# Kernel tuning notes

Measured on AMD Instinct MI355X. Metric: run time of the kernel, lower is better.

## Reference

```python
import jax, jax.numpy as jnp
import numpy as np
from jax import lax

N, CIN, H, W = 16, 3, 512, 512
BH = BW = 16  # block size (h, w); bstride == bsize so blocks tile the image
EPS = 1e-5


def setup_inputs() -> dict:
    key = jax.random.key(0)
    ks = jax.random.split(key, 32)
    def nrm(k, shape, s=0.05):
        return jax.random.normal(k, shape, jnp.float32) * s
    def bnp(k, ch):
        # rows: gamma, beta, running_mean, running_var (var kept > 0)
        u = jax.random.uniform(k, (4, ch), jnp.float32)
        return u.at[3].add(0.1)
    feat = (H // 4) * (W // 4) * 8
    return {
        "x": jax.random.normal(ks[0], (N, CIN, H, W), jnp.float32),
        "mask": jax.random.uniform(ks[1], (N, 1, H, W), jnp.float32),
        "s1_cw": nrm(ks[2], (16, CIN, 1, 1)), "s1_cb": nrm(ks[3], (16,)), "s1_bn0": bnp(ks[4], 16),
        "s1_d1w": nrm(ks[5], (32, 16, 1, 1)), "s1_d1b": nrm(ks[6], (32,)), "s1_bn1": bnp(ks[7], 32),
        "s1_d2w": nrm(ks[8], (32, 32, 3, 3)), "s1_d2b": nrm(ks[9], (32,)), "s1_bn2": bnp(ks[10], 32),
        "s1_d3w": nrm(ks[11], (16, 32, 1, 1)), "s1_d3b": nrm(ks[12], (16,)), "s1_bn3": bnp(ks[13], 16),
        "s2_cw": nrm(ks[14], (8, 16, 1, 1)), "s2_cb": nrm(ks[15], (8,)), "s2_bn0": bnp(ks[16], 8),
        "s2_d1w": nrm(ks[17], (16, 8, 1, 1)), "s2_d1b": nrm(ks[18], (16,)), "s2_bn1": bnp(ks[19], 16),
        "s2_d2w": nrm(ks[20], (16, 16, 3, 3)), "s2_d2b": nrm(ks[21], (16,)), "s2_bn2": bnp(ks[22], 16),
        "s2_d3w": nrm(ks[23], (8, 16, 1, 1)), "s2_d3b": nrm(ks[24], (8,)), "s2_bn3": bnp(ks[25], 8),
        "fc_w": nrm(ks[26], (10, feat), 0.01), "fc_b": nrm(ks[27], (10,)),
    }


def conv(x, w, b, p):
    y = lax.conv_general_dilated(x, w, (1, 1), [(p, p), (p, p)],
                                 dimension_numbers=("NCHW", "OIHW", "NCHW"))
    return y + b[None, :, None, None]


def bnorm(x, p):
    g, bt, m, v = p[0], p[1], p[2], p[3]
    scale = g * lax.rsqrt(v + EPS)
    return scale[None, :, None, None] * (x - m[None, :, None, None]) + bt[None, :, None, None]


def to_blocks(x):
    # [N,C,H,W] -> [N*nby*nbx, C, BH, BW]
    n, c, hh, ww = x.shape
    nby, nbx = hh // BH, ww // BW
    b = x.reshape(n, c, nby, BH, nbx, BW).transpose(0, 2, 4, 1, 3, 5)
    return b.reshape(n * nby * nbx, c, BH, BW), (n, nby, nbx)


def from_blocks(b, meta, c):
    n, nby, nbx = meta
    x = b.reshape(n, nby, nbx, c, BH, BW).transpose(0, 3, 1, 4, 2, 5)
    return x.reshape(n, c, nby * BH, nbx * BW)


def maxpool2(x):
    return lax.reduce_window(x, -jnp.inf, lax.max, (1, 1, 2, 2), (1, 1, 2, 2), "VALID")


def sparse_conv_block(x, mask, cw, cb, bn0, d1w, d1b, bn1, d2w, d2b, bn2, d3w, d3b, bn3):
    # reduce_mask: block is active if its mean mask value exceeds threshold
    mblocks, _ = to_blocks(mask)
    active = mblocks.mean(axis=(1, 2, 3)) > 0.5  # [N*nblocks]
    # channel path (applies to every pixel)
    xc = bnorm(jax.nn.relu(conv(x, cw, cb, 0)), bn0)
    # gather -> dense bottleneck convs per block (3x3 padded within each block) -> scatter
    blocks, meta = to_blocks(xc)
    g = bnorm(jax.nn.relu(conv(blocks, d1w, d1b, 0)), bn1)
    g = bnorm(jax.nn.relu(conv(g, d2w, d2b, 1)), bn2)
    g = bnorm(jax.nn.relu(conv(g, d3w, d3b, 0)), bn3)
    out = jnp.where(active[:, None, None, None], g, blocks)
    return from_blocks(out, meta, xc.shape[1])


def reference(x, mask, s1_cw, s1_cb, s1_bn0, s1_d1w, s1_d1b, s1_bn1, s1_d2w, s1_d2b, s1_bn2,
              s1_d3w, s1_d3b, s1_bn3, s2_cw, s2_cb, s2_bn0, s2_d1w, s2_d1b, s2_bn1,
              s2_d2w, s2_d2b, s2_bn2, s2_d3w, s2_d3b, s2_bn3, fc_w, fc_b):
    x1 = sparse_conv_block(x, mask, s1_cw, s1_cb, s1_bn0, s1_d1w, s1_d1b, s1_bn1,
                           s1_d2w, s1_d2b, s1_bn2, s1_d3w, s1_d3b, s1_bn3)
    x1 = maxpool2(x1)
    mask2 = maxpool2(mask)
    x2 = sparse_conv_block(x1, mask2, s2_cw, s2_cb, s2_bn0, s2_d1w, s2_d1b, s2_bn1,
                           s2_d2w, s2_d2b, s2_bn2, s2_d3w, s2_d3b, s2_bn3)
    x2 = maxpool2(x2)
    flat = x2.reshape(x2.shape[0], -1)  # [N, (H/4)*(W/4)*8]
    logits = flat @ fc_w.T + fc_b
    return jax.nn.softmax(logits, axis=-1)
```

## Files before the change

### kernel.cpp

```cpp
#include <hip/hip_runtime.h>
#include <math.h>


typedef __attribute__((ext_vector_type(8))) short bf16x8;
typedef __attribute__((ext_vector_type(4))) float f32x4;

#define X1P_OFF 0
#define X2_OFF  16777216
#define LG_OFF  18874368
#define P_OFF   18874624

enum : int {
  WT_S1C  = 0,
  WT_S2C  = 48,
  SC_S1BN0 = 176,
  SC_S1BN1 = 208,
  SC_S1BN2 = 272,
  SC_S1BN3 = 336,
  SC_S2BN0 = 368,
  SC_S2BN1 = 384,
  SC_S2BN2 = 416,
  SC_S2BN3 = 448,
  PH_F     = 464
};
enum : int {
  H_S1D2 = 0,
  H_S1D3 = 9216,
  H_S2D2 = 9728,
  H_S2D3 = 12288,
  H_S1D1 = 12544,
  H_S2D1 = 13568,
  PH_END = 14080
};

__device__ __forceinline__ float relu_f(float v) { return v > 0.f ? v : 0.f; }

__device__ __forceinline__ unsigned short f2bf(float f) {
  unsigned int u = __float_as_uint(f);
  unsigned int r = (u + 0x7fffu + ((u >> 16) & 1u)) >> 16;
  return (unsigned short)r;
}

__device__ __forceinline__ unsigned int pk2(float lo, float hi) {
  unsigned int r;
  asm("v_cvt_pk_bf16_f32 %0, %1, %2" : "=v"(r) : "v"(lo), "v"(hi));
  return r;
}

__device__ __forceinline__ void prep_bn(const float* __restrict__ p, int C,
                                        float* __restrict__ dst, int t) {
  for (int i = t; i < C; i += 256) {
    float g = p[i], b = p[C + i], m = p[2 * C + i], v = p[3 * C + i];
    float s = g / sqrtf(v + 1e-5f);
    dst[i] = s;
    dst[C + i] = b - s * m;
  }
}

__global__ __launch_bounds__(256) void prep_kernel(
    const float* __restrict__ s1_cw, const float* __restrict__ s1_d1w,
    const float* __restrict__ s1_d2w, const float* __restrict__ s1_d3w,
    const float* __restrict__ s2_cw, const float* __restrict__ s2_d1w,
    const float* __restrict__ s2_d2w, const float* __restrict__ s2_d3w,
    const float* __restrict__ s1_bn0, const float* __restrict__ s1_bn1,
    const float* __restrict__ s1_bn2, const float* __restrict__ s1_bn3,
    const float* __restrict__ s2_bn0, const float* __restrict__ s2_bn1,
    const float* __restrict__ s2_bn2, const float* __restrict__ s2_bn3,
    float* __restrict__ P, float* __restrict__ lg) {
  const int t = threadIdx.x;
  unsigned short* PH = (unsigned short*)(P + PH_F);
  for (int i = t; i < 48;  i += 256) { int co = i / 3,  ci = i % 3;  P[WT_S1C + ci * 16 + co] = s1_cw[i]; }
  for (int i = t; i < 128; i += 256) { int co = i / 16, ci = i % 16; P[WT_S2C + ci * 8  + co] = s2_cw[i]; }
  for (int i = t; i < 9216; i += 256) {
    int tap = i >> 10, o = (i >> 5) & 31, ci = i & 31;
    PH[H_S1D2 + i] = f2bf(s1_d2w[o * 288 + ci * 9 + tap]);
  }
  for (int i = t; i < 512; i += 256) PH[H_S1D3 + i] = f2bf(s1_d3w[i]);
  for (int i = t; i < 2560; i += 256) {
    int p = i >> 9, o = (i >> 5) & 15, k = i & 31;
    int tp = 2 * p + (k >> 4);
    PH[H_S2D2 + i] = (tp < 9) ? f2bf(s2_d2w[o * 144 + (k & 15) * 9 + tp]) : 0;
  }
  for (int i = t; i < 256; i += 256) {
    int nn = i >> 4, k = i & 15;
    PH[H_S2D3 + i] = (nn < 8) ? f2bf(s2_d3w[nn * 16 + k]) : 0;
  }
  for (int i = t; i < 1024; i += 256) {
    int o = i >> 5, k = i & 31;
    PH[H_S1D1 + i] = (k < 16) ? f2bf(s1_d1w[o * 16 + k]) : 0;
  }
  for (int i = t; i < 512; i += 256) {
    int o = i >> 5, k = i & 31;
    PH[H_S2D1 + i] = (k < 8) ? f2bf(s2_d1w[o * 8 + k]) : 0;
  }
  prep_bn(s1_bn0, 16, P + SC_S1BN0, t);
  prep_bn(s1_bn1, 32, P + SC_S1BN1, t);
  prep_bn(s1_bn2, 32, P + SC_S1BN2, t);
  prep_bn(s1_bn3, 16, P + SC_S1BN3, t);
  prep_bn(s2_bn0, 8,  P + SC_S2BN0, t);
  prep_bn(s2_bn1, 16, P + SC_S2BN1, t);
  prep_bn(s2_bn2, 16, P + SC_S2BN2, t);
  prep_bn(s2_bn3, 8,  P + SC_S2BN3, t);
  if (t < 160) lg[t] = 0.f;
}

__global__ __launch_bounds__(256, 3) void stage1_kernel(
    const float* __restrict__ x, const float* __restrict__ mask,
    const float* __restrict__ cbv, const float* __restrict__ d1b,
    const float* __restrict__ d2b, const float* __restrict__ d3b,
    const float* __restrict__ P, float* __restrict__ x1p) {
  __shared__ __align__(16) unsigned char ldsb[25920];
  __shared__ float red[4];
  __shared__ int actflag;

  const int t = threadIdx.x;
  const int ty = t >> 4, tx = t & 15;
  const int b = blockIdx.x;
  const int n = b >> 10;
  const int by = (b >> 5) & 31, bx = b & 31;
  const int gy = by * 16 + ty, gx = bx * 16 + tx;

  float s = mask[(size_t)(n * 512 + gy) * 512 + gx];
  #pragma unroll
  for (int off = 32; off > 0; off >>= 1) s += __shfl_down(s, off, 64);
  if ((t & 63) == 0) red[t >> 6] = s;
  __syncthreads();
  if (t == 0) actflag = (red[0] + red[1] + red[2] + red[3]) > 128.0f;
  __syncthreads();
  const bool active = (actflag != 0);

  float xin[3];
  #pragma unroll
  for (int c = 0; c < 3; ++c)
    xin[c] = x[(size_t)((n * 3 + c) * 512 + gy) * 512 + gx];

  const float* wc = P + WT_S1C;
  const float* sc0 = P + SC_S1BN0;
  float xc[16];
  {
    float a[16];
    #pragma unroll
    for (int o = 0; o < 16; ++o) a[o] = cbv[o];
    #pragma unroll
    for (int c = 0; c < 3; ++c) {
      const float v = xin[c];
      #pragma unroll
      for (int o = 0; o < 16; ++o) a[o] = fmaf(wc[c * 16 + o], v, a[o]);
    }
    #pragma unroll
    for (int o = 0; o < 16; ++o) xc[o] = fmaf(sc0[o], relu_f(a[o]), sc0[16 + o]);
  }

  float* const poolf = (float*)(ldsb + 20480);

  if (active) {
    const int w = t >> 6, lane = t & 63;
    const int lr = lane & 15, cb = lane >> 4;
    const unsigned short* PH = (const unsigned short*)(P + PH_F);

    if (t < 68) {
      int row, col;
      if (t < 18)      { row = 0;      col = t;      }
      else if (t < 36) { row = 17;     col = t - 18; }
      else if (t < 52) { row = t - 35; col = 0;      }
      else             { row = t - 51; col = 17;     }
      uint4* z = (uint4*)(ldsb + (row * 18 + col) * 80);
      const uint4 z4 = make_uint4(0u, 0u, 0u, 0u);
      z[0] = z4; z[1] = z4; z[2] = z4; z[3] = z4;
    }
    {
      unsigned int pk[8];
      #pragma unroll
      for (int i = 0; i < 8; ++i) pk[i] = pk2(xc[2 * i], xc[2 * i + 1]);
      uint4* dst = (uint4*)(ldsb + ((ty + 1) * 18 + (tx + 1)) * 80);
      dst[0] = make_uint4(pk[0], pk[1], pk[2], pk[3]);
      dst[1] = make_uint4(pk[4], pk[5], pk[6], pk[7]);
    }

    bf16x8 w1f[2];
    #pragma unroll
    for (int ct = 0; ct < 2; ++ct)
      w1f[ct] = *(const bf16x8*)(PH + H_S1D1 + (ct * 16 + lr) * 32 + cb * 8);
    f32x4 acc1[2][4];
    #pragma unroll
    for (int ct = 0; ct < 2; ++ct) {
      const float4 bb = *(const float4*)(d1b + ct * 16 + cb * 4);
      #pragma unroll
      for (int nt = 0; nt < 4; ++nt) {
        acc1[ct][nt][0] = bb.x; acc1[ct][nt][1] = bb.y;
        acc1[ct][nt][2] = bb.z; acc1[ct][nt][3] = bb.w;
      }
    }
    #pragma unroll
    for (int nt = 0; nt < 4; ++nt) {
      bf16x8 xcf;
      if (cb < 2) xcf = *(const bf16x8*)(ldsb + ((w * 4 + nt + 1) * 18 + lr + 1) * 80 + cb * 16);
      else        xcf = (bf16x8)(short)0;
      #pragma unroll
      for (int ct = 0; ct < 2; ++ct)
        acc1[ct][nt] = __builtin_amdgcn_mfma_f32_16x16x32_bf16(w1f[ct], xcf, acc1[ct][nt], 0, 0, 0);
    }
    #pragma unroll
    for (int ct = 0; ct < 2; ++ct) {
      const float4 s1s = *(const float4*)(P + SC_S1BN1 + ct * 16 + cb * 4);
      const float4 s1h = *(const float4*)(P + SC_S1BN1 + 32 + ct * 16 + cb * 4);
      #pragma unroll
      for (int nt = 0; nt < 4; ++nt) {
        const unsigned base = ((w * 4 + nt + 1) * 18 + lr + 1) * 80 + (ct * 16 + cb * 4) * 2;
        *(unsigned int*)(ldsb + base) =
            pk2(fmaf(s1s.x, relu_f(acc1[ct][nt][0]), s1h.x),
                fmaf(s1s.y, relu_f(acc1[ct][nt][1]), s1h.y));
        *(unsigned int*)(ldsb + base + 4) =
            pk2(fmaf(s1s.z, relu_f(acc1[ct][nt][2]), s1h.z),
                fmaf(s1s.w, relu_f(acc1[ct][nt][3]), s1h.w));
      }
    }
    __syncthreads();

    const int ct3 = w & 1, ph = w >> 1;
    bf16x8 bw[9];
    #pragma unroll
    for (int tap = 0; tap < 9; ++tap)
      bw[tap] = *(const bf16x8*)(PH + H_S1D2 + (tap * 32 + ct3 * 16 + lr) * 32 + cb * 8);
    f32x4 acc2[8];
    {
      const float4 bb = *(const float4*)(d2b + ct3 * 16 + cb * 4);
      #pragma unroll
      for (int q = 0; q < 8; ++q) {
        acc2[q][0] = bb.x; acc2[q][1] = bb.y; acc2[q][2] = bb.z; acc2[q][3] = bb.w;
      }
    }
    #pragma unroll
    for (int tap = 0; tap < 9; ++tap) {
      const int dy = tap / 3, dx = tap % 3;
      #pragma unroll
      for (int q = 0; q < 8; ++q) {
        const bf16x8 af = *(const bf16x8*)(ldsb + ((ph * 8 + q + dy) * 18 + lr + dx) * 80 + cb * 16);
        acc2[q] = __builtin_amdgcn_mfma_f32_16x16x32_bf16(bw[tap], af, acc2[q], 0, 0, 0);
      }
    }
    __syncthreads();

    {
      const float4 s2s = *(const float4*)(P + SC_S1BN2 + ct3 * 16 + cb * 4);
      const float4 s2h = *(const float4*)(P + SC_S1BN2 + 32 + ct3 * 16 + cb * 4);
      #pragma unroll
      for (int q = 0; q < 8; ++q) {
        const int pix = (ph * 8 + q) * 16 + lr;
        const unsigned base = pix * 80 + (ct3 * 16 + cb * 4) * 2;
        *(unsigned int*)(ldsb + base) =
            pk2(fmaf(s2s.x, relu_f(acc2[q][0]), s2h.x),
                fmaf(s2s.y, relu_f(acc2[q][1]), s2h.y));
        *(unsigned int*)(ldsb + base + 4) =
            pk2(fmaf(s2s.z, relu_f(acc2[q][2]), s2h.z),
                fmaf(s2s.w, relu_f(acc2[q][3]), s2h.w));
      }
    }
    __syncthreads();

    const bf16x8 b3 = *(const bf16x8*)(PH + H_S1D3 + lr * 32 + cb * 8);
    const float bias3v = d3b[lr];
    const float sc3v = P[SC_S1BN3 + lr], sh3v = P[SC_S1BN3 + 16 + lr];
    f32x4 acc3[4];
    #pragma unroll
    for (int mt = 0; mt < 4; ++mt) {
      acc3[mt][0] = bias3v; acc3[mt][1] = bias3v; acc3[mt][2] = bias3v; acc3[mt][3] = bias3v;
      const bf16x8 a3 = *(const bf16x8*)(ldsb + (w * 64 + mt * 16 + lr) * 80 + cb * 16);
      acc3[mt] = __builtin_amdgcn_mfma_f32_16x16x32_bf16(a3, b3, acc3[mt], 0, 0, 0);
    }
    #pragma unroll
    for (int mtp = 0; mtp < 2; ++mtp) {
      float o0[4], o1[4];
      #pragma unroll
      for (int r = 0; r < 4; ++r) {
        o0[r] = fmaf(sc3v, relu_f(acc3[2 * mtp][r]), sh3v);
        o1[r] = fmaf(sc3v, relu_f(acc3[2 * mtp + 1][r]), sh3v);
      }
      #pragma unroll
      for (int rp = 0; rp < 2; ++rp) {
        const float m = fmaxf(fmaxf(o0[2 * rp], o0[2 * rp + 1]),
                              fmaxf(o1[2 * rp], o1[2 * rp + 1]));
        poolf[lr * 68 + (w * 2 + mtp) * 8 + cb * 2 + rp] = m;
      }
    }
  } else {
    float* ldsf = (float*)ldsb;
    {
      float* pw = &ldsf[t * 20];
      #pragma unroll
      for (int c = 0; c < 16; ++c) pw[c] = xc[c];
    }
    __syncthreads();
    {
      const int pp = t & 63, cg = t >> 6;
      const int py = pp >> 3, px = pp & 7;
      const float* r0 = &ldsf[((2 * py) * 16 + 2 * px) * 20 + cg * 4];
      const float* r2 = &ldsf[((2 * py + 1) * 16 + 2 * px) * 20 + cg * 4];
      const float4 v0 = *(const float4*)(r0);
      const float4 v1 = *(const float4*)(r0 + 20);
      const float4 v2 = *(const float4*)(r2);
      const float4 v3 = *(const float4*)(r2 + 20);
      poolf[(cg * 4 + 0) * 68 + py * 8 + px] = fmaxf(fmaxf(v0.x, v1.x), fmaxf(v2.x, v3.x));
      poolf[(cg * 4 + 1) * 68 + py * 8 + px] = fmaxf(fmaxf(v0.y, v1.y), fmaxf(v2.y, v3.y));
      poolf[(cg * 4 + 2) * 68 + py * 8 + px] = fmaxf(fmaxf(v0.z, v1.z), fmaxf(v2.z, v3.z));
      poolf[(cg * 4 + 3) * 68 + py * 8 + px] = fmaxf(fmaxf(v0.w, v1.w), fmaxf(v2.w, v3.w));
    }
  }

  __syncthreads();
  {
    const int ch = t >> 4, idx = t & 15, yy = idx >> 1, h = idx & 1;
    const uint4 v = *(const uint4*)(poolf + ch * 68 + yy * 8 + h * 4);
    const size_t ob = ((((size_t)n * 16 + (by >> 1)) * 16 + (bx >> 1)) * 16 + ch) * 256
                      + (size_t)((by & 1) * 8 + yy) * 16 + (bx & 1) * 8 + h * 4;
    *(uint4*)(x1p + ob) = v;
  }
}

__global__ __launch_bounds__(256, 4) void stage2_kernel(
    const float* __restrict__ mask,
    const float* __restrict__ cbv, const float* __restrict__ d1b,
    const float* __restrict__ d2b, const float* __restrict__ d3b,
    const float* __restrict__ P, const float* __restrict__ x1p,
    float* __restrict__ x2) {
  __shared__ __align__(16) unsigned char ldsb2[15552];
  __shared__ float red[4];
  __shared__ int actflag;

  const int t = threadIdx.x;
  const int ty = t >> 4, tx = t & 15;
  const int b = blockIdx.x;
  const int n = b >> 8;
  const int BY = (b >> 4) & 15, BX = b & 15;

  const int my = (BY * 16 + ty) * 2, mx = (BX * 16 + tx) * 2;
  const float* mp = &mask[(size_t)(n * 512 + my) * 512 + mx];
  float s = fmaxf(fmaxf(mp[0], mp[1]), fmaxf(mp[512], mp[513]));
  #pragma unroll
  for (int off = 32; off > 0; off >>= 1) s += __shfl_down(s, off, 64);
  if ((t & 63) == 0) red[t >> 6] = s;
  __syncthreads();
  if (t == 0) actflag = (red[0] + red[1] + red[2] + red[3]) > 128.0f;
  __syncthreads();
  const bool active = (actflag != 0);

  const float* xb = x1p + (size_t)((n * 16 + BY) * 16 + BX) * 4096 + ty * 16 + tx;
  float xin[16];
  #pragma unroll
  for (int c = 0; c < 16; ++c) xin[c] = xb[c * 256];

  const float* wc = P + WT_S2C;
  const float* sc0 = P + SC_S2BN0;
  float xc[8];
  {
    float a[8];
    #pragma unroll
    for (int o = 0; o < 8; ++o) a[o] = cbv[o];
    #pragma unroll
    for (int c = 0; c < 16; ++c) {
      const float v = xin[c];
      #pragma unroll
      for (int o = 0; o < 8; ++o) a[o] = fmaf(wc[c * 8 + o], v, a[o]);
    }
    #pragma unroll
    for (int o = 0; o < 8; ++o) xc[o] = fmaf(sc0[o], relu_f(a[o]), sc0[8 + o]);
  }

  float* const poolf = (float*)(ldsb2 + 12288);

  if (active) {
    const int w = t >> 6, lane = t & 63;
    const int lr = lane & 15, cb = lane >> 4;
    const unsigned short* PH = (const unsigned short*)(P + PH_F);

    if (t < 68) {
      int row, col;
      if (t < 18)      { row = 0;      col = t;      }
      else if (t < 36) { row = 17;     col = t - 18; }
      else if (t < 52) { row = t - 35; col = 0;      }
      else             { row = t - 51; col = 17;     }
      uint4* z = (uint4*)(ldsb2 + (row * 18 + col) * 48);
      const uint4 z4 = make_uint4(0u, 0u, 0u, 0u);
      z[0] = z4; z[1] = z4;
    }
    {
      unsigned int pk[4];
      #pragma unroll
      for (int i = 0; i < 4; ++i) pk[i] = pk2(xc[2 * i], xc[2 * i + 1]);
      *(uint4*)(ldsb2 + ((ty + 1) * 18 + (tx + 1)) * 48) = make_uint4(pk[0], pk[1], pk[2], pk[3]);
    }

    const bf16x8 w1f = *(const bf16x8*)(PH + H_S2D1 + lr * 32 + cb * 8);
    f32x4 acc1[4];
    {
      const float4 bb = *(const float4*)(d1b + cb * 4);
      #pragma unroll
      for (int nt = 0; nt < 4; ++nt) {
        acc1[nt][0] = bb.x; acc1[nt][1] = bb.y; acc1[nt][2] = bb.z; acc1[nt][3] = bb.w;
      }
    }
    #pragma unroll
    for (int nt = 0; nt < 4; ++nt) {
      bf16x8 xcf;
      if (cb == 0) xcf = *(const bf16x8*)(ldsb2 + ((w * 4 + nt + 1) * 18 + lr + 1) * 48);
      else         xcf = (bf16x8)(short)0;
      acc1[nt] = __builtin_amdgcn_mfma_f32_16x16x32_bf16(w1f, xcf, acc1[nt], 0, 0, 0);
    }
    {
      const float4 s1s = *(const float4*)(P + SC_S2BN1 + cb * 4);
      const float4 s1h = *(const float4*)(P + SC_S2BN1 + 16 + cb * 4);
      #pragma unroll
      for (int nt = 0; nt < 4; ++nt) {
        const unsigned base = ((w * 4 + nt + 1) * 18 + lr + 1) * 48 + cb * 8;
        *(unsigned int*)(ldsb2 + base) =
            pk2(fmaf(s1s.x, relu_f(acc1[nt][0]), s1h.x),
                fmaf(s1s.y, relu_f(acc1[nt][1]), s1h.y));
        *(unsigned int*)(ldsb2 + base + 4) =
            pk2(fmaf(s1s.z, relu_f(acc1[nt][2]), s1h.z),
                fmaf(s1s.w, relu_f(acc1[nt][3]), s1h.w));
      }
    }
    __syncthreads();

    bf16x8 bw2[5];
    #pragma unroll
    for (int p = 0; p < 5; ++p)
      bw2[p] = *(const bf16x8*)(PH + H_S2D2 + (p * 16 + lr) * 32 + cb * 8);
    f32x4 acc2[4];
    {
      const float4 bb = *(const float4*)(d2b + cb * 4);
      #pragma unroll
      for (int nt = 0; nt < 4; ++nt) {
        acc2[nt][0] = bb.x; acc2[nt][1] = bb.y; acc2[nt][2] = bb.z; acc2[nt][3] = bb.w;
      }
    }
    #pragma unroll
    for (int p = 0; p < 5; ++p) {
      const int tp = (p < 4) ? (2 * p + (cb >> 1)) : 8;
      const int dy = (tp >= 6) ? 2 : ((tp >= 3) ? 1 : 0);
      const int dx = tp - dy * 3;
      #pragma unroll
      for (int nt = 0; nt < 4; ++nt) {
        const bf16x8 af = *(const bf16x8*)(ldsb2 + ((w * 4 + nt + dy) * 18 + lr + dx) * 48 + (cb & 1) * 16);
        acc2[nt] = __builtin_amdgcn_mfma_f32_16x16x32_bf16(bw2[p], af, acc2[nt], 0, 0, 0);
      }
    }
    __syncthreads();

    {
      const float4 s2s = *(const float4*)(P + SC_S2BN2 + cb * 4);
      const float4 s2h = *(const float4*)(P + SC_S2BN2 + 16 + cb * 4);
      #pragma unroll
      for (int nt = 0; nt < 4; ++nt) {
        const int pix = w * 64 + nt * 16 + lr;
        const unsigned base = pix * 48 + cb * 8;
        *(unsigned int*)(ldsb2 + base) =
            pk2(fmaf(s2s.x, relu_f(acc2[nt][0]), s2h.x),
                fmaf(s2s.y, relu_f(acc2[nt][1]), s2h.y));
        *(unsigned int*)(ldsb2 + base + 4) =
            pk2(fmaf(s2s.z, relu_f(acc2[nt][2]), s2h.z),
                fmaf(s2s.w, relu_f(acc2[nt][3]), s2h.w));
      }
    }
    __syncthreads();

    bf16x8 b3;
    if (cb < 2) b3 = *(const bf16x8*)(PH + H_S2D3 + lr * 16 + cb * 8);
    else        b3 = (bf16x8)(short)0;
    const float bias3v = (lr < 8) ? d3b[lr] : 0.f;
    const float sc3v = (lr < 8) ? P[SC_S2BN3 + lr] : 0.f;
    const float sh3v = (lr < 8) ? P[SC_S2BN3 + 8 + lr] : 0.f;
    f32x4 acc3[4];
    #pragma unroll
    for (int mt = 0; mt < 4; ++mt) {
      acc3[mt][0] = bias3v; acc3[mt][1] = bias3v; acc3[mt][2] = bias3v; acc3[mt][3] = bias3v;
      bf16x8 a3;
      if (cb < 2) a3 = *(const bf16x8*)(ldsb2 + (w * 64 + mt * 16 + lr) * 48 + cb * 16);
      else        a3 = (bf16x8)(short)0;
      acc3[mt] = __builtin_amdgcn_mfma_f32_16x16x32_bf16(a3, b3, acc3[mt], 0, 0, 0);
    }
    if (lr < 8) {
      #pragma unroll
      for (int mtp = 0; mtp < 2; ++mtp) {
        float o0[4], o1[4];
        #pragma unroll
        for (int r = 0; r < 4; ++r) {
          o0[r] = fmaf(sc3v, relu_f(acc3[2 * mtp][r]), sh3v);
          o1[r] = fmaf(sc3v, relu_f(acc3[2 * mtp + 1][r]), sh3v);
        }
        #pragma unroll
        for (int rp = 0; rp < 2; ++rp) {
          const float m = fmaxf(fmaxf(o0[2 * rp], o0[2 * rp + 1]),
                                fmaxf(o1[2 * rp], o1[2 * rp + 1]));
          poolf[lr * 68 + (w * 2 + mtp) * 8 + cb * 2 + rp] = m;
        }
      }
    }
  } else {
    float* ldsf = (float*)ldsb2;
    {
      float* pw = &ldsf[t * 12];
      #pragma unroll
      for (int c = 0; c < 8; ++c) pw[c] = xc[c];
    }
    __syncthreads();
    if (t < 128) {
      const int pp = t & 63, cg = t >> 6;
      const int py = pp >> 3, px = pp & 7;
      const float* r0 = &ldsf[((2 * py) * 16 + 2 * px) * 12 + cg * 4];
      const float* r2 = &ldsf[((2 * py + 1) * 16 + 2 * px) * 12 + cg * 4];
      const float4 v0 = *(const float4*)(r0);
      const float4 v1 = *(const float4*)(r0 + 12);
      const float4 v2 = *(const float4*)(r2);
      const float4 v3 = *(const float4*)(r2 + 12);
      poolf[(cg * 4 + 0) * 68 + py * 8 + px] = fmaxf(fmaxf(v0.x, v1.x), fmaxf(v2.x, v3.x));
      poolf[(cg * 4 + 1) * 68 + py * 8 + px] = fmaxf(fmaxf(v0.y, v1.y), fmaxf(v2.y, v3.y));
      poolf[(cg * 4 + 2) * 68 + py * 8 + px] = fmaxf(fmaxf(v0.z, v1.z), fmaxf(v2.z, v3.z));
      poolf[(cg * 4 + 3) * 68 + py * 8 + px] = fmaxf(fmaxf(v0.w, v1.w), fmaxf(v2.w, v3.w));
    }
  }

  __syncthreads();
  if (t < 128) {
    const int ch = t >> 4, idx = t & 15, yy = idx >> 1, h = idx & 1;
    const uint4 v = *(const uint4*)(poolf + ch * 68 + yy * 8 + h * 4);
    const size_t ob = ((size_t)(n * 8 + ch) * 128 + (BY * 8 + yy)) * 128 + BX * 8 + h * 4;
    *(uint4*)(x2 + ob) = v;
  }
}

__global__ __launch_bounds__(256) void fc_kernel(const float* __restrict__ x2,
                                                 const float* __restrict__ fcw,
                                                 const float* __restrict__ fcb,
                                                 float* __restrict__ logits) {
  __shared__ float red[4];
  const int wg = blockIdx.x, t = threadIdx.x;
  const int sp = wg & 7, k = (wg >> 3) % 10, n = wg / 80;
  const float4* xa = (const float4*)(x2 + (size_t)n * 131072) + sp * 4096;
  const float4* wa = (const float4*)(fcw + (size_t)k * 131072) + sp * 4096;
  float s = 0.f;
  #pragma unroll 4
  for (int i = t; i < 4096; i += 256) {
    const float4 a = xa[i], b = wa[i];
    s = fmaf(a.x, b.x, fmaf(a.y, b.y, fmaf(a.z, b.z, fmaf(a.w, b.w, s))));
  }
  #pragma unroll
  for (int off = 32; off > 0; off >>= 1) s += __shfl_down(s, off, 64);
  if ((t & 63) == 0) red[t >> 6] = s;
  __syncthreads();
  if (t == 0) {
    float tot = red[0] + red[1] + red[2] + red[3];
    if (sp == 0) tot += fcb[k];
    atomicAdd(&logits[n * 10 + k], tot);
  }
}

__global__ void softmax_kernel(const float* __restrict__ logits, float* __restrict__ out) {
  const int t = threadIdx.x;
  if (t < 16) {
    float l[10], mx = -1e30f;
    #pragma unroll
    for (int k = 0; k < 10; ++k) { l[k] = logits[t * 10 + k]; mx = fmaxf(mx, l[k]); }
    float sum = 0.f;
    #pragma unroll
    for (int k = 0; k < 10; ++k) { l[k] = expf(l[k] - mx); sum += l[k]; }
    const float inv = 1.f / sum;
    #pragma unroll
    for (int k = 0; k < 10; ++k) out[t * 10 + k] = l[k] * inv;
  }
}

extern "C" void kernel_launch(void* const* d_in, const int* in_sizes, int n_in,
                              void* d_out, int out_size, void* d_ws, size_t ws_size,
                              hipStream_t stream) {
  const float* x      = (const float*)d_in[0];
  const float* mask   = (const float*)d_in[1];
  const float* s1_cw  = (const float*)d_in[2];
  const float* s1_cb  = (const float*)d_in[3];
  const float* s1_bn0 = (const float*)d_in[4];
  const float* s1_d1w = (const float*)d_in[5];
  const float* s1_d1b = (const float*)d_in[6];
  const float* s1_bn1 = (const float*)d_in[7];
  const float* s1_d2w = (const float*)d_in[8];
  const float* s1_d2b = (const float*)d_in[9];
  const float* s1_bn2 = (const float*)d_in[10];
  const float* s1_d3w = (const float*)d_in[11];
  const float* s1_d3b = (const float*)d_in[12];
  const float* s1_bn3 = (const float*)d_in[13];
  const float* s2_cw  = (const float*)d_in[14];
  const float* s2_cb  = (const float*)d_in[15];
  const float* s2_bn0 = (const float*)d_in[16];
  const float* s2_d1w = (const float*)d_in[17];
  const float* s2_d1b = (const float*)d_in[18];
  const float* s2_bn1 = (const float*)d_in[19];
  const float* s2_d2w = (const float*)d_in[20];
  const float* s2_d2b = (const float*)d_in[21];
  const float* s2_bn2 = (const float*)d_in[22];
  const float* s2_d3w = (const float*)d_in[23];
  const float* s2_d3b = (const float*)d_in[24];
  const float* s2_bn3 = (const float*)d_in[25];
  const float* fc_w   = (const float*)d_in[26];
  const float* fc_b   = (const float*)d_in[27];

  float* ws  = (float*)d_ws;
  float* x1p = ws + X1P_OFF;
  float* x2  = ws + X2_OFF;
  float* lg  = ws + LG_OFF;
  float* P   = ws + P_OFF;

  prep_kernel<<<1, 256, 0, stream>>>(s1_cw, s1_d1w, s1_d2w, s1_d3w,
                                     s2_cw, s2_d1w, s2_d2w, s2_d3w,
                                     s1_bn0, s1_bn1, s1_bn2, s1_bn3,
                                     s2_bn0, s2_bn1, s2_bn2, s2_bn3, P, lg);
  stage1_kernel<<<16 * 32 * 32, 256, 0, stream>>>(x, mask, s1_cb, s1_d1b, s1_d2b, s1_d3b, P, x1p);
  stage2_kernel<<<16 * 16 * 16, 256, 0, stream>>>(mask, s2_cb, s2_d1b, s2_d2b, s2_d3b, P, x1p, x2);
  fc_kernel<<<1280, 256, 0, stream>>>(x2, fc_w, fc_b, lg);
  softmax_kernel<<<1, 64, 0, stream>>>(lg, (float*)d_out);
}
```

Baseline: 295.4 us.

## Precompute stage-2 activity sums in stage 1 and cut register pressure for occupancy

Stage 1 now also computes the 2x2-maxpooled mask sum for each stage-2 block and accumulates it with atomics into a small buffer zeroed by the prep kernel. Stage 2 reads that one value instead of re-reading the mask and running its own block reduction and two barriers. The 3x3 conv weight loads are moved inside non-unrolled per-row (stage 1) and per-pair (stage 2) loops, and launch bounds are raised to 4 and 5 blocks per CU. The cost is fewer live registers and higher occupancy, traded for repeated weight loads inside the loop, atomics, and less unrolling.

```diff
diff --git a/kernel.cpp b/kernel.cpp
--- a/kernel.cpp
+++ b/kernel.cpp
@@ -8,7 +8,8 @@
 #define X1P_OFF 0
 #define X2_OFF  16777216
 #define LG_OFF  18874368
-#define P_OFF   18874624
+#define MS_OFF  18874624
+#define P_OFF   18878720
 
 enum : int {
   WT_S1C  = 0,
@@ -66,7 +67,7 @@
     const float* __restrict__ s1_bn2, const float* __restrict__ s1_bn3,
     const float* __restrict__ s2_bn0, const float* __restrict__ s2_bn1,
     const float* __restrict__ s2_bn2, const float* __restrict__ s2_bn3,
-    float* __restrict__ P, float* __restrict__ lg) {
+    float* __restrict__ P, float* __restrict__ lg, float* __restrict__ ms) {
   const int t = threadIdx.x;
   unsigned short* PH = (unsigned short*)(P + PH_F);
   for (int i = t; i < 48;  i += 256) { int co = i / 3,  ci = i % 3;  P[WT_S1C + ci * 16 + co] = s1_cw[i]; }
@@ -102,16 +103,17 @@
   prep_bn(s2_bn2, 16, P + SC_S2BN2, t);
   prep_bn(s2_bn3, 8,  P + SC_S2BN3, t);
   if (t < 160) lg[t] = 0.f;
-}
-
-__global__ __launch_bounds__(256, 3) void stage1_kernel(
+  for (int i = t; i < 4096; i += 256) ms[i] = 0.f;
+}
+
+__global__ __launch_bounds__(256, 4) void stage1_kernel(
     const float* __restrict__ x, const float* __restrict__ mask,
     const float* __restrict__ cbv, const float* __restrict__ d1b,
     const float* __restrict__ d2b, const float* __restrict__ d3b,
-    const float* __restrict__ P, float* __restrict__ x1p) {
+    const float* __restrict__ P, float* __restrict__ x1p,
+    float* __restrict__ msum) {
   __shared__ __align__(16) unsigned char ldsb[25920];
-  __shared__ float red[4];
-  __shared__ int actflag;
+  __shared__ float red_s[4], red_v[4];
 
   const int t = threadIdx.x;
   const int ty = t >> 4, tx = t & 15;
@@ -120,14 +122,19 @@
   const int by = (b >> 5) & 31, bx = b & 31;
   const int gy = by * 16 + ty, gx = bx * 16 + tx;
 
-  float s = mask[(size_t)(n * 512 + gy) * 512 + gx];
-  #pragma unroll
-  for (int off = 32; off > 0; off >>= 1) s += __shfl_down(s, off, 64);
-  if ((t & 63) == 0) red[t >> 6] = s;
+  {
+    const float m = mask[(size_t)(n * 512 + gy) * 512 + gx];
+    float v = fmaxf(m, __shfl_xor(m, 1, 64));
+    v = fmaxf(v, __shfl_xor(v, 16, 64));
+    float s = m;
+    #pragma unroll
+    for (int off = 32; off > 0; off >>= 1) {
+      s += __shfl_down(s, off, 64);
+      v += __shfl_down(v, off, 64);
+    }
+    if ((t & 63) == 0) { red_s[t >> 6] = s; red_v[t >> 6] = v; }
+  }
   __syncthreads();
-  if (t == 0) actflag = (red[0] + red[1] + red[2] + red[3]) > 128.0f;
-  __syncthreads();
-  const bool active = (actflag != 0);
 
   float xin[3];
   #pragma unroll
@@ -150,6 +157,11 @@
     #pragma unroll
     for (int o = 0; o < 16; ++o) xc[o] = fmaf(sc0[o], relu_f(a[o]), sc0[16 + o]);
   }
+
+  const bool active = (red_s[0] + red_s[1] + red_s[2] + red_s[3]) > 128.0f;
+  if (t == 0)
+    atomicAdd(&msum[n * 256 + (by >> 1) * 16 + (bx >> 1)],
+              (red_v[0] + red_v[1] + red_v[2] + red_v[3]) * 0.25f);
 
   float* const poolf = (float*)(ldsb + 20480);
 
@@ -177,51 +189,49 @@
       dst[1] = make_uint4(pk[4], pk[5], pk[6], pk[7]);
     }
 
-    bf16x8 w1f[2];
-    #pragma unroll
-    for (int ct = 0; ct < 2; ++ct)
-      w1f[ct] = *(const bf16x8*)(PH + H_S1D1 + (ct * 16 + lr) * 32 + cb * 8);
-    f32x4 acc1[2][4];
-    #pragma unroll
-    for (int ct = 0; ct < 2; ++ct) {
-      const float4 bb = *(const float4*)(d1b + ct * 16 + cb * 4);
+    {
+      bf16x8 w1f[2];
+      #pragma unroll
+      for (int ct = 0; ct < 2; ++ct)
+        w1f[ct] = *(const bf16x8*)(PH + H_S1D1 + (ct * 16 + lr) * 32 + cb * 8);
+      f32x4 acc1[2][4];
+      #pragma unroll
+      for (int ct = 0; ct < 2; ++ct) {
+        const float4 bb = *(const float4*)(d1b + ct * 16 + cb * 4);
+        #pragma unroll
+        for (int nt = 0; nt < 4; ++nt) {
+          acc1[ct][nt][0] = bb.x; acc1[ct][nt][1] = bb.y;
+          acc1[ct][nt][2] = bb.z; acc1[ct][nt][3] = bb.w;
+        }
+      }
       #pragma unroll
       for (int nt = 0; nt < 4; ++nt) {
-        acc1[ct][nt][0] = bb.x; acc1[ct][nt][1] = bb.y;
-        acc1[ct][nt][2] = bb.z; acc1[ct][nt][3] = bb.w;
-      }
-    }
-    #pragma unroll
-    for (int nt = 0; nt < 4; ++nt) {
-      bf16x8 xcf;
-      if (cb < 2) xcf = *(const bf16x8*)(ldsb + ((w * 4 + nt + 1) * 18 + lr + 1) * 80 + cb * 16);
-      else        xcf = (bf16x8)(short)0;
-      #pragma unroll
-      for (int ct = 0; ct < 2; ++ct)
-        acc1[ct][nt] = __builtin_amdgcn_mfma_f32_16x16x32_bf16(w1f[ct], xcf, acc1[ct][nt], 0, 0, 0);
-    }
-    #pragma unroll
-    for (int ct = 0; ct < 2; ++ct) {
-      const float4 s1s = *(const float4*)(P + SC_S1BN1 + ct * 16 + cb * 4);
-      const float4 s1h = *(const float4*)(P + SC_S1BN1 + 32 + ct * 16 + cb * 4);
-      #pragma unroll
-      for (int nt = 0; nt < 4; ++nt) {
-        const unsigned base = ((w * 4 + nt + 1) * 18 + lr + 1) * 80 + (ct * 16 + cb * 4) * 2;
-        *(unsigned int*)(ldsb + base) =
-            pk2(fmaf(s1s.x, relu_f(acc1[ct][nt][0]), s1h.x),
-                fmaf(s1s.y, relu_f(acc1[ct][nt][1]), s1h.y));
-        *(unsigned int*)(ldsb + base + 4) =
-            pk2(fmaf(s1s.z, relu_f(acc1[ct][nt][2]), s1h.z),
-                fmaf(s1s.w, relu_f(acc1[ct][nt][3]), s1h.w));
+        bf16x8 xcf;
+        if (cb < 2) xcf = *(const bf16x8*)(ldsb + ((w * 4 + nt + 1) * 18 + lr + 1) * 80 + cb * 16);
+        else        xcf = (bf16x8)(short)0;
+        #pragma unroll
+        for (int ct = 0; ct < 2; ++ct)
+          acc1[ct][nt] = __builtin_amdgcn_mfma_f32_16x16x32_bf16(w1f[ct], xcf, acc1[ct][nt], 0, 0, 0);
+      }
+      #pragma unroll
+      for (int ct = 0; ct < 2; ++ct) {
+        const float4 s1s = *(const float4*)(P + SC_S1BN1 + ct * 16 + cb * 4);
+        const float4 s1h = *(const float4*)(P + SC_S1BN1 + 32 + ct * 16 + cb * 4);
+        #pragma unroll
+        for (int nt = 0; nt < 4; ++nt) {
+          const unsigned base = ((w * 4 + nt + 1) * 18 + lr + 1) * 80 + (ct * 16 + cb * 4) * 2;
+          *(unsigned int*)(ldsb + base) =
+              pk2(fmaf(s1s.x, relu_f(acc1[ct][nt][0]), s1h.x),
+                  fmaf(s1s.y, relu_f(acc1[ct][nt][1]), s1h.y));
+          *(unsigned int*)(ldsb + base + 4) =
+              pk2(fmaf(s1s.z, relu_f(acc1[ct][nt][2]), s1h.z),
+                  fmaf(s1s.w, relu_f(acc1[ct][nt][3]), s1h.w));
+        }
       }
     }
     __syncthreads();
 
     const int ct3 = w & 1, ph = w >> 1;
-    bf16x8 bw[9];
-    #pragma unroll
-    for (int tap = 0; tap < 9; ++tap)
-      bw[tap] = *(const bf16x8*)(PH + H_S1D2 + (tap * 32 + ct3 * 16 + lr) * 32 + cb * 8);
     f32x4 acc2[8];
     {
       const float4 bb = *(const float4*)(d2b + ct3 * 16 + cb * 4);
@@ -230,14 +240,20 @@
         acc2[q][0] = bb.x; acc2[q][1] = bb.y; acc2[q][2] = bb.z; acc2[q][3] = bb.w;
       }
     }
-    #pragma unroll
-    for (int tap = 0; tap < 9; ++tap) {
-      const int dy = tap / 3, dx = tap % 3;
-      #pragma unroll
-      for (int q = 0; q < 8; ++q) {
-        const bf16x8 af = *(const bf16x8*)(ldsb + ((ph * 8 + q + dy) * 18 + lr + dx) * 80 + cb * 16);
-        acc2[q] = __builtin_amdgcn_mfma_f32_16x16x32_bf16(bw[tap], af, acc2[q], 0, 0, 0);
-      }
+    #pragma clang loop unroll(disable)
+    for (int dy = 0; dy < 3; ++dy) {
+      bf16x8 bwr[3];
+      #pragma unroll
+      for (int dx = 0; dx < 3; ++dx)
+        bwr[dx] = *(const bf16x8*)(PH + H_S1D2 + ((dy * 3 + dx) * 32 + ct3 * 16 + lr) * 32 + cb * 8);
+      const int rb = (ph * 8 + dy) * 18 + lr;
+      #pragma unroll
+      for (int dx = 0; dx < 3; ++dx)
+        #pragma unroll
+        for (int q = 0; q < 8; ++q) {
+          const bf16x8 af = *(const bf16x8*)(ldsb + (rb + q * 18 + dx) * 80 + cb * 16);
+          acc2[q] = __builtin_amdgcn_mfma_f32_16x16x32_bf16(bwr[dx], af, acc2[q], 0, 0, 0);
+        }
     }
     __syncthreads();
 
@@ -317,15 +333,13 @@
   }
 }
 
-__global__ __launch_bounds__(256, 4) void stage2_kernel(
-    const float* __restrict__ mask,
+__global__ __launch_bounds__(256, 5) void stage2_kernel(
+    const float* __restrict__ msum,
     const float* __restrict__ cbv, const float* __restrict__ d1b,
     const float* __restrict__ d2b, const float* __restrict__ d3b,
     const float* __restrict__ P, const float* __restrict__ x1p,
     float* __restrict__ x2) {
   __shared__ __align__(16) unsigned char ldsb2[15552];
-  __shared__ float red[4];
-  __shared__ int actflag;
 
   const int t = threadIdx.x;
   const int ty = t >> 4, tx = t & 15;
@@ -333,18 +347,9 @@
   const int n = b >> 8;
   const int BY = (b >> 4) & 15, BX = b & 15;
 
-  const int my = (BY * 16 + ty) * 2, mx = (BX * 16 + tx) * 2;
-  const float* mp = &mask[(size_t)(n * 512 + my) * 512 + mx];
-  float s = fmaxf(fmaxf(mp[0], mp[1]), fmaxf(mp[512], mp[513]));
-  #pragma unroll
-  for (int off = 32; off > 0; off >>= 1) s += __shfl_down(s, off, 64);
-  if ((t & 63) == 0) red[t >> 6] = s;
-  __syncthreads();
-  if (t == 0) actflag = (red[0] + red[1] + red[2] + red[3]) > 128.0f;
-  __syncthreads();
-  const bool active = (actflag != 0);
-
-  const float* xb = x1p + (size_t)((n * 16 + BY) * 16 + BX) * 4096 + ty * 16 + tx;
+  const bool active = msum[b] > 128.0f;
+
+  const float* xb = x1p + (size_t)b * 4096 + ty * 16 + tx;
   float xin[16];
   #pragma unroll
   for (int c = 0; c < 16; ++c) xin[c] = xb[c * 256];
@@ -390,42 +395,40 @@
       *(uint4*)(ldsb2 + ((ty + 1) * 18 + (tx + 1)) * 48) = make_uint4(pk[0], pk[1], pk[2], pk[3]);
     }
 
-    const bf16x8 w1f = *(const bf16x8*)(PH + H_S2D1 + lr * 32 + cb * 8);
-    f32x4 acc1[4];
-    {
-      const float4 bb = *(const float4*)(d1b + cb * 4);
+    {
+      const bf16x8 w1f = *(const bf16x8*)(PH + H_S2D1 + lr * 32 + cb * 8);
+      f32x4 acc1[4];
+      {
+        const float4 bb = *(const float4*)(d1b + cb * 4);
+        #pragma unroll
+        for (int nt = 0; nt < 4; ++nt) {
+          acc1[nt][0] = bb.x; acc1[nt][1] = bb.y; acc1[nt][2] = bb.z; acc1[nt][3] = bb.w;
+        }
+      }
       #pragma unroll
       for (int nt = 0; nt < 4; ++nt) {
-        acc1[nt][0] = bb.x; acc1[nt][1] = bb.y; acc1[nt][2] = bb.z; acc1[nt][3] = bb.w;
-      }
-    }
-    #pragma unroll
-    for (int nt = 0; nt < 4; ++nt) {
-      bf16x8 xcf;
-      if (cb == 0) xcf = *(const bf16x8*)(ldsb2 + ((w * 4 + nt + 1) * 18 + lr + 1) * 48);
-      else         xcf = (bf16x8)(short)0;
-      acc1[nt] = __builtin_amdgcn_mfma_f32_16x16x32_bf16(w1f, xcf, acc1[nt], 0, 0, 0);
-    }
-    {
-      const float4 s1s = *(const float4*)(P + SC_S2BN1 + cb * 4);
-      const float4 s1h = *(const float4*)(P + SC_S2BN1 + 16 + cb * 4);
-      #pragma unroll
-      for (int nt = 0; nt < 4; ++nt) {
-        const unsigned base = ((w * 4 + nt + 1) * 18 + lr + 1) * 48 + cb * 8;
-        *(unsigned int*)(ldsb2 + base) =
-            pk2(fmaf(s1s.x, relu_f(acc1[nt][0]), s1h.x),
-                fmaf(s1s.y, relu_f(acc1[nt][1]), s1h.y));
-        *(unsigned int*)(ldsb2 + base + 4) =
-            pk2(fmaf(s1s.z, relu_f(acc1[nt][2]), s1h.z),
-                fmaf(s1s.w, relu_f(acc1[nt][3]), s1h.w));
-      }
-    }
-    __syncthreads();
-
-    bf16x8 bw2[5];
-    #pragma unroll
-    for (int p = 0; p < 5; ++p)
-      bw2[p] = *(const bf16x8*)(PH + H_S2D2 + (p * 16 + lr) * 32 + cb * 8);
+        bf16x8 xcf;
+        if (cb == 0) xcf = *(const bf16x8*)(ldsb2 + ((w * 4 + nt + 1) * 18 + lr + 1) * 48);
+        else         xcf = (bf16x8)(short)0;
+        acc1[nt] = __builtin_amdgcn_mfma_f32_16x16x32_bf16(w1f, xcf, acc1[nt], 0, 0, 0);
+      }
+      {
+        const float4 s1s = *(const float4*)(P + SC_S2BN1 + cb * 4);
+        const float4 s1h = *(const float4*)(P + SC_S2BN1 + 16 + cb * 4);
+        #pragma unroll
+        for (int nt = 0; nt < 4; ++nt) {
+          const unsigned base = ((w * 4 + nt + 1) * 18 + lr + 1) * 48 + cb * 8;
+          *(unsigned int*)(ldsb2 + base) =
+              pk2(fmaf(s1s.x, relu_f(acc1[nt][0]), s1h.x),
+                  fmaf(s1s.y, relu_f(acc1[nt][1]), s1h.y));
+          *(unsigned int*)(ldsb2 + base + 4) =
+              pk2(fmaf(s1s.z, relu_f(acc1[nt][2]), s1h.z),
+                  fmaf(s1s.w, relu_f(acc1[nt][3]), s1h.w));
+        }
+      }
+    }
+    __syncthreads();
+
     f32x4 acc2[4];
     {
       const float4 bb = *(const float4*)(d2b + cb * 4);
@@ -434,15 +437,16 @@
         acc2[nt][0] = bb.x; acc2[nt][1] = bb.y; acc2[nt][2] = bb.z; acc2[nt][3] = bb.w;
       }
     }
-    #pragma unroll
+    #pragma clang loop unroll(disable)
     for (int p = 0; p < 5; ++p) {
+      const bf16x8 bwp = *(const bf16x8*)(PH + H_S2D2 + (p * 16 + lr) * 32 + cb * 8);
       const int tp = (p < 4) ? (2 * p + (cb >> 1)) : 8;
       const int dy = (tp >= 6) ? 2 : ((tp >= 3) ? 1 : 0);
       const int dx = tp - dy * 3;
       #pragma unroll
       for (int nt = 0; nt < 4; ++nt) {
         const bf16x8 af = *(const bf16x8*)(ldsb2 + ((w * 4 + nt + dy) * 18 + lr + dx) * 48 + (cb & 1) * 16);
-        acc2[nt] = __builtin_amdgcn_mfma_f32_16x16x32_bf16(bw2[p], af, acc2[nt], 0, 0, 0);
+        acc2[nt] = __builtin_amdgcn_mfma_f32_16x16x32_bf16(bwp, af, acc2[nt], 0, 0, 0);
       }
     }
     __syncthreads();
@@ -606,14 +610,15 @@
   float* x1p = ws + X1P_OFF;
   float* x2  = ws + X2_OFF;
   float* lg  = ws + LG_OFF;
+  float* ms  = ws + MS_OFF;
   float* P   = ws + P_OFF;
 
   prep_kernel<<<1, 256, 0, stream>>>(s1_cw, s1_d1w, s1_d2w, s1_d3w,
                                      s2_cw, s2_d1w, s2_d2w, s2_d3w,
                                      s1_bn0, s1_bn1, s1_bn2, s1_bn3,
-                                     s2_bn0, s2_bn1, s2_bn2, s2_bn3, P, lg);
-  stage1_kernel<<<16 * 32 * 32, 256, 0, stream>>>(x, mask, s1_cb, s1_d1b, s1_d2b, s1_d3b, P, x1p);
-  stage2_kernel<<<16 * 16 * 16, 256, 0, stream>>>(mask, s2_cb, s2_d1b, s2_d2b, s2_d3b, P, x1p, x2);
+                                     s2_bn0, s2_bn1, s2_bn2, s2_bn3, P, lg, ms);
+  stage1_kernel<<<16 * 32 * 32, 256, 0, stream>>>(x, mask, s1_cb, s1_d1b, s1_d2b, s1_d3b, P, x1p, ms);
+  stage2_kernel<<<16 * 16 * 16, 256, 0, stream>>>(ms, s2_cb, s2_d1b, s2_d2b, s2_d3b, P, x1p, x2);
   fc_kernel<<<1280, 256, 0, stream>>>(x2, fc_w, fc_b, lg);
   softmax_kernel<<<1, 64, 0, stream>>>(lg, (float*)d_out);
 }
```

Measured after the change: 284.7 us. -3.6%, faster.
